# Kernel tuning notes

Hardware: AMD Instinct MI355X
Metric: run time of the kernel (lower is better)

## Reference

```python
import jax, jax.numpy as jnp
import numpy as np

HS = 4096   # hidden_size
IS = 2048   # input_size (also number of output classes)
T, B = 4, 1 # seq_len * batch MUST equal 4 (output.view(4,-1) constraint)


def setup_inputs() -> dict:
    key = jax.random.key(0)
    ks = jax.random.split(key, 5)
    inp = jax.random.normal(ks[0], (T, B, IS), dtype=jnp.float32)
    target = jax.random.randint(ks[1], (T * B, 1), 0, IS)
    # xavier-style init for 2D params, zeros for bias-like (per init_weights)
    weight = jax.random.normal(ks[2], (4 * HS, IS + HS), dtype=jnp.float32) * np.float32(1.0 / np.sqrt(IS + HS))
    bias = jnp.zeros((4 * HS, 1), dtype=jnp.float32)
    W = jax.random.normal(ks[3], (IS, HS), dtype=jnp.float32) * np.float32(1.0 / np.sqrt(HS))
    b = jnp.zeros((IS, 1), dtype=jnp.float32)
    return {"input": inp, "target": target, "weight": weight, "bias": bias, "W": W, "b": b}


def reference(input, target, weight, bias, W, b):
    hs = weight.shape[0] // 4
    seq_len, batch, _ = input.shape
    h0 = jnp.zeros((hs, batch), dtype=input.dtype)
    c0 = jnp.zeros((hs, batch), dtype=input.dtype)

    def step(carry, x_t):
        h, c = carry
        z = jnp.concatenate([h, x_t.T], axis=0)          # [HS+IS, B]
        g = weight @ z + bias                            # [4*HS, B]
        f = jax.nn.sigmoid(g[:hs])
        i = jax.nn.sigmoid(g[hs:2 * hs])
        c_bar = jnp.tanh(g[2 * hs:3 * hs])
        o = jax.nn.sigmoid(g[3 * hs:])
        c = c * f + c_bar * i
        h = jnp.tanh(c) * o
        return (h, c), h

    _, outs = jax.lax.scan(step, (h0, c0), input)        # outs: [T, HS, B]
    # transpose(2,1) then view(4,-1): valid only when T*B == 4
    out = outs.transpose(0, 2, 1).reshape(4, -1)          # [4, HS]
    logits = (W @ out.T + b).T                            # [4, IS]
    logp = jax.nn.log_softmax(logits, axis=1)             # stable softmax+log
    rows = jnp.arange(logits.shape[0])
    # loss = sum over rows of -log softmax at target class (scatter one-hot * pred)
    loss = -jnp.sum(logp[rows, target[:, 0]])
    return loss
```

## Files before the change

### kernel.cpp

```cpp
#include <hip/hip_runtime.h>
#include <math.h>

#define HS 4096
#define IS 2048
#define NT 4
#define NR 16384
#define ZD 6144

__device__ __forceinline__ float wave_reduce(float v) {
#pragma unroll
    for (int off = 32; off > 0; off >>= 1) v += __shfl_xor(v, off, 64);
    return v;
}

__device__ __forceinline__ float sigf(float x) { return 1.0f / (1.0f + expf(-x)); }

__global__ __launch_bounds__(256) void gx_kernel(
    const float* __restrict__ x,
    const float* __restrict__ weight,
    const float* __restrict__ bias,
    float* __restrict__ Gx)
{
    __shared__ float xs[NT * IS];
    const int tid = threadIdx.x;
    for (int i = tid; i < NT * IS; i += 256) xs[i] = x[i];
    __syncthreads();

    const int wave = tid >> 6, lane = tid & 63;
    const int r = blockIdx.x * 4 + wave;
    const float4* wrow = reinterpret_cast<const float4*>(weight + (size_t)r * ZD + HS);
    const float4* xs4 = reinterpret_cast<const float4*>(xs);

    float a0 = 0.f, a1 = 0.f, a2 = 0.f, a3 = 0.f;
#pragma unroll
    for (int it = 0; it < (IS / 4) / 64; ++it) {
        const int e = it * 64 + lane;
        const float4 w = wrow[e];
        const float4 p = xs4[e];
        const float4 q = xs4[(IS / 4) + e];
        const float4 s = xs4[2 * (IS / 4) + e];
        const float4 u = xs4[3 * (IS / 4) + e];
        a0 += w.x * p.x + w.y * p.y + w.z * p.z + w.w * p.w;
        a1 += w.x * q.x + w.y * q.y + w.z * q.z + w.w * q.w;
        a2 += w.x * s.x + w.y * s.y + w.z * s.z + w.w * s.w;
        a3 += w.x * u.x + w.y * u.y + w.z * u.z + w.w * u.w;
    }
    a0 = wave_reduce(a0); a1 = wave_reduce(a1);
    a2 = wave_reduce(a2); a3 = wave_reduce(a3);
    if (lane == 0) {
        const float bb = bias[r];
        Gx[0 * NR + r] = a0 + bb;
        Gx[1 * NR + r] = a1 + bb;
        Gx[2 * NR + r] = a2 + bb;
        Gx[3 * NR + r] = a3 + bb;
    }
}

__global__ __launch_bounds__(256) void step0_kernel(
    const float* __restrict__ Gx,
    float* __restrict__ H0,
    float* __restrict__ cvec)
{
    const int j = blockIdx.x * 256 + threadIdx.x;
    const float gi = Gx[HS + j];
    const float gc = Gx[2 * HS + j];
    const float go = Gx[3 * HS + j];
    const float cn = tanhf(gc) * sigf(gi);
    cvec[j] = cn;
    H0[j] = tanhf(cn) * sigf(go);
}

__global__ __launch_bounds__(256) void steph_kernel(
    const float* __restrict__ weight,
    const float* __restrict__ Gx,
    const float* __restrict__ Hprev,
    float* __restrict__ Hout,
    float* __restrict__ cvec,
    const int t)
{
    __shared__ float hs_[HS];
    const int tid = threadIdx.x;
    for (int i = tid; i < HS; i += 256) hs_[i] = Hprev[i];
    __syncthreads();

    const int wave = tid >> 6, lane = tid & 63;
    const int j = blockIdx.x * 4 + wave;
    const float4* h4 = reinterpret_cast<const float4*>(hs_);

    float acc[4];
#pragma unroll
    for (int k = 0; k < 4; ++k) {
        const float4* wrow = reinterpret_cast<const float4*>(weight + (size_t)(k * HS + j) * ZD);
        float a = 0.f;
#pragma unroll
        for (int it = 0; it < (HS / 4) / 64; ++it) {
            const int e = it * 64 + lane;
            const float4 w = wrow[e];
            const float4 h = h4[e];
            a += w.x * h.x + w.y * h.y + w.z * h.z + w.w * h.w;
        }
        acc[k] = a;
    }
#pragma unroll
    for (int k = 0; k < 4; ++k) acc[k] = wave_reduce(acc[k]);

    if (lane == 0) {
        const size_t gb = (size_t)t * NR;
        const float gf = acc[0] + Gx[gb + j];
        const float gi = acc[1] + Gx[gb + HS + j];
        const float gc = acc[2] + Gx[gb + 2 * HS + j];
        const float go = acc[3] + Gx[gb + 3 * HS + j];
        const float cn = cvec[j] * sigf(gf) + tanhf(gc) * sigf(gi);
        cvec[j] = cn;
        Hout[j] = tanhf(cn) * sigf(go);
    }
}

__global__ __launch_bounds__(256) void logits_kernel(
    const float* __restrict__ W,
    const float* __restrict__ bvec,
    const float* __restrict__ H,
    float* __restrict__ logits)
{
    const int wave = threadIdx.x >> 6, lane = threadIdx.x & 63;
    const int r = blockIdx.x * 4 + wave;
    const float4* wrow = reinterpret_cast<const float4*>(W + (size_t)r * HS);
    const float4* H4 = reinterpret_cast<const float4*>(H);

    float acc[4] = {0.f, 0.f, 0.f, 0.f};
#pragma unroll
    for (int it = 0; it < (HS / 4) / 64; ++it) {
        const int e = it * 64 + lane;
        const float4 w = wrow[e];
#pragma unroll
        for (int t = 0; t < 4; ++t) {
            const float4 h = H4[t * (HS / 4) + e];
            acc[t] += w.x * h.x + w.y * h.y + w.z * h.z + w.w * h.w;
        }
    }
#pragma unroll
    for (int t = 0; t < 4; ++t) acc[t] = wave_reduce(acc[t]);
    if (lane == 0) {
        const float bv = bvec[r];
#pragma unroll
        for (int t = 0; t < 4; ++t) logits[t * IS + r] = acc[t] + bv;
    }
}

__global__ __launch_bounds__(256) void loss_kernel(
    const float* __restrict__ logits,
    const int* __restrict__ target,
    float* __restrict__ out)
{
    __shared__ float red[256];
    const int tid = threadIdx.x;
    float total = 0.f;
    for (int t = 0; t < NT; ++t) {
        const float* row = logits + t * IS;
        float m = -1e30f;
        for (int r = tid; r < IS; r += 256) m = fmaxf(m, row[r]);
        red[tid] = m;
        __syncthreads();
        for (int s = 128; s > 0; s >>= 1) {
            if (tid < s) red[tid] = fmaxf(red[tid], red[tid + s]);
            __syncthreads();
        }
        m = red[0];
        __syncthreads();
        float sum = 0.f;
        for (int r = tid; r < IS; r += 256) sum += expf(row[r] - m);
        red[tid] = sum;
        __syncthreads();
        for (int s = 128; s > 0; s >>= 1) {
            if (tid < s) red[tid] += red[tid + s];
            __syncthreads();
        }
        if (tid == 0) {
            const float lse = m + logf(red[0]);
            total += lse - row[target[t]];
        }
        __syncthreads();
    }
    if (tid == 0) out[0] = total;
}

extern "C" void kernel_launch(void* const* d_in, const int* in_sizes, int n_in,
                              void* d_out, int out_size, void* d_ws, size_t ws_size,
                              hipStream_t stream) {
    const float* x      = (const float*)d_in[0];
    const int*   target = (const int*)  d_in[1];
    const float* weight = (const float*)d_in[2];
    const float* bias   = (const float*)d_in[3];
    const float* W      = (const float*)d_in[4];
    const float* bvec   = (const float*)d_in[5];
    float* out = (float*)d_out;

    float* ws = (float*)d_ws;
    float* Gx     = ws;
    float* H      = ws + 65536;
    float* cvec   = ws + 65536 + 16384;
    float* logits = ws + 65536 + 16384 + 4096;

    hipLaunchKernelGGL(gx_kernel, dim3(NR / 4), dim3(256), 0, stream, x, weight, bias, Gx);
    hipLaunchKernelGGL(step0_kernel, dim3(HS / 256), dim3(256), 0, stream, Gx, H, cvec);
    for (int t = 1; t < NT; ++t) {
        hipLaunchKernelGGL(steph_kernel, dim3(HS / 4), dim3(256), 0, stream,
                           weight, Gx, H + (size_t)(t - 1) * HS, H + (size_t)t * HS, cvec, t);
    }
    hipLaunchKernelGGL(logits_kernel, dim3(IS / 4), dim3(256), 0, stream, W, bvec, H, logits);
    hipLaunchKernelGGL(loss_kernel, dim3(1), dim3(256), 0, stream, logits, target, out);
}
```

Measured before the change: 192.4 us.

## Convert recurrent weights to fp16 during first step and reuse for later steps

The first recurrent step reads the fp32 recurrent weight block and also writes an fp16 copy to workspace. The remaining two steps read that fp16 copy instead, halving their weight traffic. In exchange the first step does an extra 128MB write, and later steps lose precision in the weights. All of the conversion happens inside the timed call, so nothing is reused across calls.

```diff
diff --git a/kernel.cpp b/kernel.cpp
--- a/kernel.cpp
+++ b/kernel.cpp
@@ -6,6 +6,8 @@
 #define NT 4
 #define NR 16384
 #define ZD 6144
+
+typedef _Float16 f16;
 
 __device__ __forceinline__ float wave_reduce(float v) {
 #pragma unroll
@@ -70,13 +72,13 @@
     H0[j] = tanhf(cn) * sigf(go);
 }
 
-__global__ __launch_bounds__(256) void steph_kernel(
+__global__ __launch_bounds__(256) void steph_conv_kernel(
     const float* __restrict__ weight,
     const float* __restrict__ Gx,
     const float* __restrict__ Hprev,
     float* __restrict__ Hout,
     float* __restrict__ cvec,
-    const int t)
+    f16* __restrict__ Whb)
 {
     __shared__ float hs_[HS];
     const int tid = threadIdx.x;
@@ -90,7 +92,9 @@
     float acc[4];
 #pragma unroll
     for (int k = 0; k < 4; ++k) {
-        const float4* wrow = reinterpret_cast<const float4*>(weight + (size_t)(k * HS + j) * ZD);
+        const int row = k * HS + j;
+        const float4* wrow = reinterpret_cast<const float4*>(weight + (size_t)row * ZD);
+        uint2* wout = reinterpret_cast<uint2*>(Whb + (size_t)row * HS);
         float a = 0.f;
 #pragma unroll
         for (int it = 0; it < (HS / 4) / 64; ++it) {
@@ -98,6 +102,62 @@
             const float4 w = wrow[e];
             const float4 h = h4[e];
             a += w.x * h.x + w.y * h.y + w.z * h.z + w.w * h.w;
+            union { f16 hv[4]; uint2 u; } pk;
+            pk.hv[0] = (f16)w.x; pk.hv[1] = (f16)w.y;
+            pk.hv[2] = (f16)w.z; pk.hv[3] = (f16)w.w;
+            wout[e] = pk.u;
+        }
+        acc[k] = a;
+    }
+#pragma unroll
+    for (int k = 0; k < 4; ++k) acc[k] = wave_reduce(acc[k]);
+
+    if (lane == 0) {
+        const size_t gb = (size_t)1 * NR;
+        const float gf = acc[0] + Gx[gb + j];
+        const float gi = acc[1] + Gx[gb + HS + j];
+        const float gc = acc[2] + Gx[gb + 2 * HS + j];
+        const float go = acc[3] + Gx[gb + 3 * HS + j];
+        const float cn = cvec[j] * sigf(gf) + tanhf(gc) * sigf(gi);
+        cvec[j] = cn;
+        Hout[j] = tanhf(cn) * sigf(go);
+    }
+}
+
+__global__ __launch_bounds__(256) void steph_f16_kernel(
+    const f16* __restrict__ Whb,
+    const float* __restrict__ Gx,
+    const float* __restrict__ Hprev,
+    float* __restrict__ Hout,
+    float* __restrict__ cvec,
+    const int t)
+{
+    __shared__ float hs_[HS];
+    const int tid = threadIdx.x;
+    for (int i = tid; i < HS; i += 256) hs_[i] = Hprev[i];
+    __syncthreads();
+
+    const int wave = tid >> 6, lane = tid & 63;
+    const int j = blockIdx.x * 4 + wave;
+    const float4* h4 = reinterpret_cast<const float4*>(hs_);
+
+    float acc[4];
+#pragma unroll
+    for (int k = 0; k < 4; ++k) {
+        const int row = k * HS + j;
+        const uint4* wrow = reinterpret_cast<const uint4*>(Whb + (size_t)row * HS);
+        float a = 0.f;
+#pragma unroll
+        for (int it = 0; it < (HS / 8) / 64; ++it) {
+            const int e = it * 64 + lane;
+            union { uint4 u; f16 hv[8]; } wv;
+            wv.u = wrow[e];
+            const float4 ha = h4[2 * e];
+            const float4 hb = h4[2 * e + 1];
+            a += (float)wv.hv[0] * ha.x + (float)wv.hv[1] * ha.y
+               + (float)wv.hv[2] * ha.z + (float)wv.hv[3] * ha.w
+               + (float)wv.hv[4] * hb.x + (float)wv.hv[5] * hb.y
+               + (float)wv.hv[6] * hb.z + (float)wv.hv[7] * hb.w;
         }
         acc[k] = a;
     }
@@ -195,18 +255,21 @@
     const float* bvec   = (const float*)d_in[5];
     float* out = (float*)d_out;
 
-    float* ws = (float*)d_ws;
-    float* Gx     = ws;
-    float* H      = ws + 65536;
-    float* cvec   = ws + 65536 + 16384;
-    float* logits = ws + 65536 + 16384 + 4096;
+    f16*   Whb = (f16*)d_ws;
+    float* fws = (float*)((char*)d_ws + (size_t)NR * HS * sizeof(f16));
+    float* Gx     = fws;
+    float* H      = fws + 65536;
+    float* cvec   = fws + 65536 + 16384;
+    float* logits = fws + 65536 + 16384 + 4096;
 
     hipLaunchKernelGGL(gx_kernel, dim3(NR / 4), dim3(256), 0, stream, x, weight, bias, Gx);
     hipLaunchKernelGGL(step0_kernel, dim3(HS / 256), dim3(256), 0, stream, Gx, H, cvec);
-    for (int t = 1; t < NT; ++t) {
-        hipLaunchKernelGGL(steph_kernel, dim3(HS / 4), dim3(256), 0, stream,
-                           weight, Gx, H + (size_t)(t - 1) * HS, H + (size_t)t * HS, cvec, t);
-    }
+    hipLaunchKernelGGL(steph_conv_kernel, dim3(HS / 4), dim3(256), 0, stream,
+                       weight, Gx, H, H + HS, cvec, Whb);
+    hipLaunchKernelGGL(steph_f16_kernel, dim3(HS / 4), dim3(256), 0, stream,
+                       Whb, Gx, H + HS, H + 2 * HS, cvec, 2);
+    hipLaunchKernelGGL(steph_f16_kernel, dim3(HS / 4), dim3(256), 0, stream,
+                       Whb, Gx, H + 2 * HS, H + 3 * HS, cvec, 3);
     hipLaunchKernelGGL(logits_kernel, dim3(IS / 4), dim3(256), 0, stream, W, bvec, H, logits);
     hipLaunchKernelGGL(loss_kernel, dim3(1), dim3(256), 0, stream, logits, target, out);
 }
```

New measurement: 206.8 us. 1.07x slower.

## Quantize recurrent weights to FP8 on first step and reuse for later LSTM steps

Applied to the files above, without the earlier changes.

The first recurrent step still reads the fp32 hidden-weight block. While doing so it also writes an FP8 (e4m3) packed copy of that block to workspace. The last two recurrent steps read the FP8 copy, which is a quarter of the bytes, and unpack it to fp32 for the dot products, so each of those steps moves much less memory. Weight streams in the gx, step and logits kernels now use nontemporal loads. The cost is an extra 64MB write during the first step and FP8 rounding error in the weights for two of the steps, which may break tolerance.

```diff
diff --git a/kernel.cpp b/kernel.cpp
--- a/kernel.cpp
+++ b/kernel.cpp
@@ -7,13 +7,20 @@
 #define NR 16384
 #define ZD 6144
 
+typedef float fvec4 __attribute__((ext_vector_type(4)));
+typedef float ef2 __attribute__((ext_vector_type(2)));
+
 __device__ __forceinline__ float wave_reduce(float v) {
 #pragma unroll
     for (int off = 32; off > 0; off >>= 1) v += __shfl_xor(v, off, 64);
     return v;
 }
-
 __device__ __forceinline__ float sigf(float x) { return 1.0f / (1.0f + expf(-x)); }
+
+static __device__ __forceinline__ float4 ldnt(const float4* p) {
+    fvec4 v = __builtin_nontemporal_load(reinterpret_cast<const fvec4*>(p));
+    return make_float4(v.x, v.y, v.z, v.w);
+}
 
 __global__ __launch_bounds__(256) void gx_kernel(
     const float* __restrict__ x,
@@ -35,7 +42,7 @@
 #pragma unroll
     for (int it = 0; it < (IS / 4) / 64; ++it) {
         const int e = it * 64 + lane;
-        const float4 w = wrow[e];
+        const float4 w = ldnt(&wrow[e]);
         const float4 p = xs4[e];
         const float4 q = xs4[(IS / 4) + e];
         const float4 s = xs4[2 * (IS / 4) + e];
@@ -70,17 +77,21 @@
     H0[j] = tanhf(cn) * sigf(go);
 }
 
-__global__ __launch_bounds__(256) void steph_kernel(
+__global__ __launch_bounds__(256) void steph_conv_kernel(
     const float* __restrict__ weight,
     const float* __restrict__ Gx,
     const float* __restrict__ Hprev,
     float* __restrict__ Hout,
     float* __restrict__ cvec,
-    const int t)
-{
-    __shared__ float hs_[HS];
-    const int tid = threadIdx.x;
-    for (int i = tid; i < HS; i += 256) hs_[i] = Hprev[i];
+    unsigned int* __restrict__ Whb8)
+{
+    __shared__ __align__(16) float hs_[HS];
+    const int tid = threadIdx.x;
+    {
+        const float4* hp4 = reinterpret_cast<const float4*>(Hprev);
+        float4* hb4 = reinterpret_cast<float4*>(hs_);
+        for (int i = tid; i < HS / 4; i += 256) hb4[i] = hp4[i];
+    }
     __syncthreads();
 
     const int wave = tid >> 6, lane = tid & 63;
@@ -90,14 +101,19 @@
     float acc[4];
 #pragma unroll
     for (int k = 0; k < 4; ++k) {
-        const float4* wrow = reinterpret_cast<const float4*>(weight + (size_t)(k * HS + j) * ZD);
+        const int row = k * HS + j;
+        const float4* wrow = reinterpret_cast<const float4*>(weight + (size_t)row * ZD);
+        unsigned int* wout = Whb8 + (size_t)row * 1024;
         float a = 0.f;
 #pragma unroll
-        for (int it = 0; it < (HS / 4) / 64; ++it) {
+        for (int it = 0; it < 16; ++it) {
             const int e = it * 64 + lane;
-            const float4 w = wrow[e];
+            const float4 w = ldnt(&wrow[e]);
             const float4 h = h4[e];
             a += w.x * h.x + w.y * h.y + w.z * h.z + w.w * h.w;
+            int u = __builtin_amdgcn_cvt_pk_fp8_f32(w.x, w.y, 0, false);
+            u = __builtin_amdgcn_cvt_pk_fp8_f32(w.z, w.w, u, true);
+            wout[e] = (unsigned int)u;
         }
         acc[k] = a;
     }
@@ -105,7 +121,7 @@
     for (int k = 0; k < 4; ++k) acc[k] = wave_reduce(acc[k]);
 
     if (lane == 0) {
-        const size_t gb = (size_t)t * NR;
+        const size_t gb = (size_t)1 * NR;
         const float gf = acc[0] + Gx[gb + j];
         const float gi = acc[1] + Gx[gb + HS + j];
         const float gc = acc[2] + Gx[gb + 2 * HS + j];
@@ -116,6 +132,77 @@
     }
 }
 
+__global__ __launch_bounds__(256) void steph_fp8_kernel(
+    const unsigned int* __restrict__ Whb8,
+    const float* __restrict__ Gx,
+    const float* __restrict__ Hprev,
+    float* __restrict__ Hout,
+    float* __restrict__ cvec,
+    const int t)
+{
+    __shared__ __align__(16) float hs_[HS];
+    const int tid = threadIdx.x;
+    {
+        const float4* hp4 = reinterpret_cast<const float4*>(Hprev);
+        float4* hb4 = reinterpret_cast<float4*>(hs_);
+        for (int i = tid; i < HS / 4; i += 256) hb4[i] = hp4[i];
+    }
+    __syncthreads();
+
+    const int wave = tid >> 6, lane = tid & 63;
+    const int j = blockIdx.x * 4 + wave;
+    const float4* h4 = reinterpret_cast<const float4*>(hs_);
+
+    const unsigned int* w0 = Whb8 + (size_t)(0 * HS + j) * 1024;
+    const unsigned int* w1 = Whb8 + (size_t)(1 * HS + j) * 1024;
+    const unsigned int* w2 = Whb8 + (size_t)(2 * HS + j) * 1024;
+    const unsigned int* w3 = Whb8 + (size_t)(3 * HS + j) * 1024;
+
+    float a0 = 0.f, a1 = 0.f, a2 = 0.f, a3 = 0.f;
+#pragma unroll
+    for (int it = 0; it < 16; ++it) {
+        const int e = it * 64 + lane;
+        const float4 h = h4[e];
+        {
+            const int u = (int)w0[e];
+            const ef2 lo = __builtin_amdgcn_cvt_pk_f32_fp8(u, false);
+            const ef2 hi = __builtin_amdgcn_cvt_pk_f32_fp8(u, true);
+            a0 += lo.x * h.x + lo.y * h.y + hi.x * h.z + hi.y * h.w;
+        }
+        {
+            const int u = (int)w1[e];
+            const ef2 lo = __builtin_amdgcn_cvt_pk_f32_fp8(u, false);
+            const ef2 hi = __builtin_amdgcn_cvt_pk_f32_fp8(u, true);
+            a1 += lo.x * h.x + lo.y * h.y + hi.x * h.z + hi.y * h.w;
+        }
+        {
+            const int u = (int)w2[e];
+            const ef2 lo = __builtin_amdgcn_cvt_pk_f32_fp8(u, false);
+            const ef2 hi = __builtin_amdgcn_cvt_pk_f32_fp8(u, true);
+            a2 += lo.x * h.x + lo.y * h.y + hi.x * h.z + hi.y * h.w;
+        }
+        {
+            const int u = (int)w3[e];
+            const ef2 lo = __builtin_amdgcn_cvt_pk_f32_fp8(u, false);
+            const ef2 hi = __builtin_amdgcn_cvt_pk_f32_fp8(u, true);
+            a3 += lo.x * h.x + lo.y * h.y + hi.x * h.z + hi.y * h.w;
+        }
+    }
+    a0 = wave_reduce(a0); a1 = wave_reduce(a1);
+    a2 = wave_reduce(a2); a3 = wave_reduce(a3);
+
+    if (lane == 0) {
+        const size_t gb = (size_t)t * NR;
+        const float gf = a0 + Gx[gb + j];
+        const float gi = a1 + Gx[gb + HS + j];
+        const float gc = a2 + Gx[gb + 2 * HS + j];
+        const float go = a3 + Gx[gb + 3 * HS + j];
+        const float cn = cvec[j] * sigf(gf) + tanhf(gc) * sigf(gi);
+        cvec[j] = cn;
+        Hout[j] = tanhf(cn) * sigf(go);
+    }
+}
+
 __global__ __launch_bounds__(256) void logits_kernel(
     const float* __restrict__ W,
     const float* __restrict__ bvec,
@@ -129,9 +216,9 @@
 
     float acc[4] = {0.f, 0.f, 0.f, 0.f};
 #pragma unroll
-    for (int it = 0; it < (HS / 4) / 64; ++it) {
+    for (int it = 0; it < 16; ++it) {
         const int e = it * 64 + lane;
-        const float4 w = wrow[e];
+        const float4 w = ldnt(&wrow[e]);
 #pragma unroll
         for (int t = 0; t < 4; ++t) {
             const float4 h = H4[t * (HS / 4) + e];
@@ -156,7 +243,7 @@
     const int tid = threadIdx.x;
     float total = 0.f;
     for (int t = 0; t < NT; ++t) {
-        const float* row = logits + t * IS;
+        const float* row = logits + (size_t)t * IS;
         float m = -1e30f;
         for (int r = tid; r < IS; r += 256) m = fmaxf(m, row[r]);
         red[tid] = m;
@@ -175,10 +262,7 @@
             if (tid < s) red[tid] += red[tid + s];
             __syncthreads();
         }
-        if (tid == 0) {
-            const float lse = m + logf(red[0]);
-            total += lse - row[target[t]];
-        }
+        if (tid == 0) total += (m + logf(red[0])) - row[target[t]];
         __syncthreads();
     }
     if (tid == 0) out[0] = total;
@@ -195,18 +279,21 @@
     const float* bvec   = (const float*)d_in[5];
     float* out = (float*)d_out;
 
-    float* ws = (float*)d_ws;
-    float* Gx     = ws;
-    float* H      = ws + 65536;
-    float* cvec   = ws + 65536 + 16384;
-    float* logits = ws + 65536 + 16384 + 4096;
+    unsigned int* Whb8 = (unsigned int*)d_ws;
+    float* fws = (float*)((char*)d_ws + (size_t)NR * 1024 * 4);
+    float* Gx     = fws;
+    float* H      = fws + 65536;
+    float* cvec   = fws + 65536 + 16384;
+    float* logits = fws + 65536 + 16384 + 4096;
 
     hipLaunchKernelGGL(gx_kernel, dim3(NR / 4), dim3(256), 0, stream, x, weight, bias, Gx);
     hipLaunchKernelGGL(step0_kernel, dim3(HS / 256), dim3(256), 0, stream, Gx, H, cvec);
-    for (int t = 1; t < NT; ++t) {
-        hipLaunchKernelGGL(steph_kernel, dim3(HS / 4), dim3(256), 0, stream,
-                           weight, Gx, H + (size_t)(t - 1) * HS, H + (size_t)t * HS, cvec, t);
-    }
+    hipLaunchKernelGGL(steph_conv_kernel, dim3(HS / 4), dim3(256), 0, stream,
+                       weight, Gx, H, H + HS, cvec, Whb8);
+    hipLaunchKernelGGL(steph_fp8_kernel, dim3(HS / 4), dim3(256), 0, stream,
+                       Whb8, Gx, H + HS, H + 2 * HS, cvec, 2);
+    hipLaunchKernelGGL(steph_fp8_kernel, dim3(HS / 4), dim3(256), 0, stream,
+                       Whb8, Gx, H + 2 * HS, H + 3 * HS, cvec, 3);
     hipLaunchKernelGGL(logits_kernel, dim3(IS / 4), dim3(256), 0, stream, W, bvec, H, logits);
     hipLaunchKernelGGL(loss_kernel, dim3(1), dim3(256), 0, stream, logits, target, out);
 }
```

After: 197.2 us. 1.02x slower.
